# Performance work log

Measured on AMD Instinct MI355X. Metric: run time of the kernel, lower is better.

## Reference

```python
import jax, jax.numpy as jnp
import numpy as np

N, E = 20000, 320000
IN_DIM, CODE_DIM, HIDDEN, HEADS, NREL = 896, 768, 256, 4, 5
CH = HIDDEN // HEADS
CODE_WEIGHT = 3.0
NEG_SLOPE = 0.2


def _gat_layer(h, src, dst, W, att_src, att_dst, bias):
    # h: [N, HIDDEN]; src/dst already include self-loops. Eval mode -> no dropout.
    n = h.shape[0]
    x = (h @ W).reshape(n, HEADS, CH)                      # [N,H,C]
    a_src = (x * att_src).sum(-1)                          # [N,H]
    a_dst = (x * att_dst).sum(-1)                          # [N,H]
    alpha = jax.nn.leaky_relu(a_src[src] + a_dst[dst], NEG_SLOPE)  # [E',H]
    amax = jax.ops.segment_max(alpha, dst, num_segments=n)
    amax = jnp.where(jnp.isfinite(amax), amax, 0.0)
    ex = jnp.exp(alpha - amax[dst])
    denom = jax.ops.segment_sum(ex, dst, num_segments=n)
    coef = ex / denom[dst]                                 # segment softmax over in-neighbors
    msg = x[src] * coef[:, :, None]                        # [E',H,C]
    out = jax.ops.segment_sum(msg, dst, num_segments=n)    # [N,H,C]
    return out.reshape(n, HEADS * CH) + bias


def setup_inputs() -> dict:
    key = jax.random.key(0)
    ks = jax.random.split(key, 20)
    def glorot(k, shape):
        fan_in = shape[0]
        return jax.random.normal(k, shape, jnp.float32) / jnp.sqrt(jnp.asarray(fan_in, jnp.float32))
    inp = {
        "x": jax.random.normal(ks[0], (N, IN_DIM), jnp.float32),
        "edge_index": jax.random.randint(ks[1], (2, E), 0, N, jnp.int32),
        "edge_type": jax.random.randint(ks[2], (E,), 0, NREL, jnp.int32),
        "edge_weight": jax.random.uniform(ks[3], (E,), jnp.float32),
        "rel_emb": jax.random.normal(ks[4], (NREL, HIDDEN), jnp.float32),
        "Wp": glorot(ks[5], (IN_DIM, HIDDEN)),
        "bp": jnp.zeros((HIDDEN,), jnp.float32),
        "W1": glorot(ks[6], (HIDDEN, HIDDEN)),
        "att_src1": glorot(ks[7], (HEADS, CH)) * 0.1,
        "att_dst1": glorot(ks[8], (HEADS, CH)) * 0.1,
        "b1": jnp.zeros((HIDDEN,), jnp.float32),
        "W2": glorot(ks[9], (HIDDEN, HIDDEN)),
        "att_src2": glorot(ks[10], (HEADS, CH)) * 0.1,
        "att_dst2": glorot(ks[11], (HEADS, CH)) * 0.1,
        "b2": jnp.zeros((HIDDEN,), jnp.float32),
        "Wo": glorot(ks[12], (HIDDEN, 1)),
        "bo": jnp.zeros((1,), jnp.float32),
    }
    return inp


def reference(x, edge_index, edge_type, edge_weight, rel_emb, Wp, bp,
              W1, att_src1, att_dst1, b1, W2, att_src2, att_dst2, b2, Wo, bo):
    # feature reorder + code reweighting
    x_code = x[:, :CODE_DIM]
    x_num = x[:, CODE_DIM:]
    xc = jnp.concatenate([x_num, CODE_WEIGHT * x_code], axis=-1)
    h = jax.nn.relu(xc @ Wp + bp)                          # [N,HIDDEN]

    src, dst = edge_index[0], edge_index[1]
    # relational message + index_add scatter
    rel = rel_emb[edge_type] * edge_weight[:, None]        # [E,HIDDEN]
    msg = h[src] + rel
    h = h + jax.ops.segment_sum(msg, dst, num_segments=N)

    # GATConv adds self-loops by default
    loop = jnp.arange(N, dtype=src.dtype)
    src_sl = jnp.concatenate([src, loop])
    dst_sl = jnp.concatenate([dst, loop])

    h = _gat_layer(h, src_sl, dst_sl, W1, att_src1, att_dst1, b1)
    h = _gat_layer(h, src_sl, dst_sl, W2, att_src2, att_dst2, b2)
    score = (h @ Wo + bo)[:, 0]                            # [N]
    return score
```

## Files before the change

### kernel.cpp

```cpp
#include <hip/hip_runtime.h>
#include <hip/hip_bf16.h>

#define N_NODES 20000
#define E_EDGES 320000

typedef __attribute__((ext_vector_type(8))) short s8v;
typedef __attribute__((ext_vector_type(4))) float f4v;

__device__ __forceinline__ float lrelu(float v){ return v > 0.f ? v : 0.2f * v; }

__device__ __forceinline__ float bitf(unsigned short u){
  union { unsigned int i; float f; } v; v.i = ((unsigned int)u) << 16; return v.f;
}
__device__ __forceinline__ float4 bf4(const unsigned short* p){
  ushort4 u = *(const ushort4*)p;
  return make_float4(bitf(u.x), bitf(u.y), bitf(u.z), bitf(u.w));
}
__device__ __forceinline__ unsigned short bfhi(float v){
  union{float f; unsigned u;} a; a.f = v;
  unsigned r = a.u + 0x7FFFu + ((a.u >> 16) & 1u);
  return (unsigned short)(r >> 16);
}
__device__ __forceinline__ float bf2f(unsigned short h){
  union{unsigned u; float f;} a; a.u = ((unsigned)h) << 16; return a.f;
}
__device__ __forceinline__ void split2(float v0, float v1, unsigned& hu, unsigned& lu){
  __hip_bfloat162 h2 = __float22bfloat162_rn(make_float2(v0, v1));
  unsigned h; __builtin_memcpy(&h, &h2, 4);
  union{unsigned u; float f;} c0, c1;
  c0.u = h << 16;
  c1.u = h & 0xFFFF0000u;
  __hip_bfloat162 l2 = __float22bfloat162_rn(make_float2(v0 - c0.f, v1 - c1.f));
  unsigned l; __builtin_memcpy(&l, &l2, 4);
  hu = h; lu = l;
}
__device__ __forceinline__ void gl_lds16(const void* g, void* l){
  __builtin_amdgcn_global_load_lds(
      (const __attribute__((address_space(1))) unsigned int*)g,
      (__attribute__((address_space(3))) unsigned int*)l, 16, 0, 0);
}

__global__ __launch_bounds__(256) void k_count(const int* __restrict__ dst, int* __restrict__ deg, int E){
  int e = blockIdx.x * 256 + threadIdx.x;
  if (e < E) atomicAdd(&deg[dst[e]], 1);
}

__global__ __launch_bounds__(256) void k_scan(const int* __restrict__ deg, int* __restrict__ off,
                                              int* __restrict__ cur, int n){
  __shared__ int part[256];
  __shared__ int base[257];
  int tid = threadIdx.x;
  int chunk = (n + 255) / 256;
  int st = tid * chunk;
  int en = st + chunk; if (en > n) en = n;
  int s = 0;
  for (int i = st; i < en; ++i) s += deg[i];
  part[tid] = s;
  __syncthreads();
  if (tid == 0){
    int a = 0;
    for (int i = 0; i < 256; ++i){ base[i] = a; a += part[i]; }
    base[256] = a;
  }
  __syncthreads();
  int a = base[tid];
  for (int i = st; i < en; ++i){ off[i] = a; cur[i] = 0; a += deg[i]; }
  if (tid == 0) off[n] = base[256];
}

__global__ __launch_bounds__(256) void k_fill(const int* __restrict__ src, const int* __restrict__ dst,
                       const int* __restrict__ ety, const float* __restrict__ ew,
                       const int* __restrict__ off, int* __restrict__ cur,
                       int* __restrict__ csrc, int* __restrict__ cet, float* __restrict__ cw, int E){
  int e = blockIdx.x * 256 + threadIdx.x;
  if (e < E){
    int d = dst[e];
    int p = atomicAdd(&cur[d], 1);
    int i = off[d] + p;
    csrc[i] = src[e];
    cet[i]  = ety[e];
    cw[i]   = ew[e];
  }
}

template<bool SC3>
__global__ __launch_bounds__(64) void k_prep(const float* __restrict__ W, unsigned short* __restrict__ Bp, int K){
  int kt = blockIdx.x;
  int n  = blockIdx.y * 64 + threadIdx.x;
  unsigned short hi[32], lo[32];
#pragma unroll
  for (int kk = 0; kk < 32; ++kk){
    int krow = kt * 32 + kk;
    float v = W[(size_t)krow * 256 + n];
    if constexpr (SC3){ if (krow >= 128) v *= 3.0f; }
    unsigned short h = bfhi(v);
    hi[kk] = h;
    lo[kk] = bfhi(v - bf2f(h));
  }
  size_t plane = (size_t)(K >> 5) * 256 * 32;
  size_t b = ((size_t)kt * 256 + n) * 32;
#pragma unroll
  for (int kk = 0; kk < 32; ++kk){
    Bp[b + kk]         = hi[kk];
    Bp[plane + b + kk] = lo[kk];
  }
}

template<int KT, bool ARAW, bool EPI, bool ATT, bool CBF>
__global__ __launch_bounds__(256, 2) void k_mm(
    const float* __restrict__ Araw,
    const unsigned short* __restrict__ Ahi, const unsigned short* __restrict__ Alo,
    const unsigned short* __restrict__ Bp,
    const float* __restrict__ bias, void* __restrict__ Cout,
    const float* __restrict__ attS, const float* __restrict__ attD,
    float* __restrict__ aS, float* __restrict__ aD)
{
  constexpr int TILE = ARAW ? 8192 : 4096;
  __shared__ alignas(16) unsigned char Abuf[2][TILE];

  const int tid  = threadIdx.x;
  const int lane = tid & 63;
  const int w    = tid >> 6;
  const int l15  = lane & 15;
  const int kg   = lane >> 4;
  const int m0   = blockIdx.x * 32;
  const size_t planeB = (size_t)KT * 256 * 32;

  f4v acc[2][4];
#pragma unroll
  for (int f = 0; f < 2; ++f)
#pragma unroll
    for (int g = 0; g < 4; ++g)
#pragma unroll
      for (int r = 0; r < 4; ++r) acc[f][g][r] = 0.f;

  auto stage = [&](int buf, int kt){
    if constexpr (ARAW){
#pragma unroll
      for (int seg = 0; seg < 2; ++seg){
        int s   = seg * 256 + tid;
        int row = s >> 3;
        int jj  = s & 7;
        int kcp = jj >> 1, h = jj & 1;
        int kc  = kcp ^ (row & 3);
        int c   = kt * 32 + kc * 8 + h * 4;
        int xcol = (c < 128) ? (768 + c) : (c - 128);
        const float* gp = Araw + (size_t)(m0 + row) * 896 + xcol;
        gl_lds16(gp, &Abuf[buf][seg * 4096 + w * 1024]);
      }
    } else {
      int s   = tid;
      int p   = s >> 7;
      int sp  = s & 127;
      int row = sp >> 2;
      int kcp = sp & 3;
      int kc  = kcp ^ (row & 3);
      const unsigned short* basep = p ? Alo : Ahi;
      const unsigned short* gp = basep + (size_t)(m0 + row) * 256 + kt * 32 + kc * 8;
      gl_lds16(gp, &Abuf[buf][w * 1024]);
    }
  };

  auto readFrags = [&](s8v* ah, s8v* al, int buf){
#pragma unroll
    for (int f = 0; f < 2; ++f){
      int row = f * 16 + l15;
      int kc  = kg ^ (row & 3);
      if constexpr (ARAW){
        const unsigned char* p0 = &Abuf[buf][row * 128 + kc * 32];
        float4 x0 = *(const float4*)p0;
        float4 x1 = *(const float4*)(p0 + 16);
        union{unsigned u[4]; s8v s;} H, L;
        split2(x0.x, x0.y, H.u[0], L.u[0]);
        split2(x0.z, x0.w, H.u[1], L.u[1]);
        split2(x1.x, x1.y, H.u[2], L.u[2]);
        split2(x1.z, x1.w, H.u[3], L.u[3]);
        ah[f] = H.s; al[f] = L.s;
      } else {
        ah[f] = *(const s8v*)&Abuf[buf][row * 64 + kc * 16];
        al[f] = *(const s8v*)&Abuf[buf][2048 + row * 64 + kc * 16];
      }
    }
  };

  auto loadB = [&](s8v* bh, s8v* bl, int kt){
#pragma unroll
    for (int g = 0; g < 4; ++g){
      const unsigned short* bp2 = Bp + ((size_t)kt * 256 + w * 64 + g * 16 + l15) * 32 + kg * 8;
      bh[g] = *(const s8v*)bp2;
      bl[g] = *(const s8v*)(bp2 + planeB);
    }
  };

  auto doMFMA = [&](const s8v* ah, const s8v* al, const s8v* bh, const s8v* bl){
#pragma unroll
    for (int f = 0; f < 2; ++f)
#pragma unroll
      for (int g = 0; g < 4; ++g){
        acc[f][g] = __builtin_amdgcn_mfma_f32_16x16x32_bf16(ah[f], bh[g], acc[f][g], 0, 0, 0);
        acc[f][g] = __builtin_amdgcn_mfma_f32_16x16x32_bf16(ah[f], bl[g], acc[f][g], 0, 0, 0);
        acc[f][g] = __builtin_amdgcn_mfma_f32_16x16x32_bf16(al[f], bh[g], acc[f][g], 0, 0, 0);
      }
  };

  s8v bh[4], bl[4];
  stage(0, 0);
  loadB(bh, bl, 0);
  __syncthreads();

  int cur = 0;
#pragma unroll 1
  for (int kt = 0; kt < KT; ++kt){
    if (kt + 1 < KT) stage(cur ^ 1, kt + 1);
    s8v ah[2], al[2];
    readFrags(ah, al, cur);
    s8v nbh[4], nbl[4];
    if (kt + 1 < KT) loadB(nbh, nbl, kt + 1);
    doMFMA(ah, al, bh, bl);
    if (kt + 1 < KT){
#pragma unroll
      for (int g = 0; g < 4; ++g){ bh[g] = nbh[g]; bl[g] = nbl[g]; }
    }
    __syncthreads();
    cur ^= 1;
  }

#pragma unroll
  for (int f = 0; f < 2; ++f){
#pragma unroll
    for (int g = 0; g < 4; ++g){
      int col = w * 64 + g * 16 + l15;
      float bb = EPI ? bias[col] : 0.f;
#pragma unroll
      for (int r = 0; r < 4; ++r){
        int row = m0 + f * 16 + kg * 4 + r;
        float v = acc[f][g][r];
        if constexpr (EPI) v = fmaxf(v + bb, 0.f);
        if constexpr (CBF) ((unsigned short*)Cout)[(size_t)row * 256 + col] = bfhi(v);
        else               ((float*)Cout)[(size_t)row * 256 + col] = v;
      }
    }
  }

  if constexpr (ATT){
    const int head = w;
    float sv[4], dv[4];
#pragma unroll
    for (int g = 0; g < 4; ++g){
      int col = w * 64 + g * 16 + l15;
      sv[g] = attS[col];
      dv[g] = attD[col];
    }
#pragma unroll
    for (int f = 0; f < 2; ++f){
#pragma unroll
      for (int r = 0; r < 4; ++r){
        float ps = acc[f][0][r]*sv[0] + acc[f][1][r]*sv[1] + acc[f][2][r]*sv[2] + acc[f][3][r]*sv[3];
        float pd = acc[f][0][r]*dv[0] + acc[f][1][r]*dv[1] + acc[f][2][r]*dv[2] + acc[f][3][r]*dv[3];
#pragma unroll
        for (int mm = 1; mm < 16; mm <<= 1){
          ps += __shfl_xor(ps, mm, 64);
          pd += __shfl_xor(pd, mm, 64);
        }
        int row = m0 + f * 16 + kg * 4 + r;
        if (l15 == 0){
          aS[(size_t)row * 4 + head] = ps;
          aD[(size_t)row * 4 + head] = pd;
        }
      }
    }
  }
}

__global__ __launch_bounds__(256) void k_agg(
    const unsigned short* __restrict__ h0, const int* __restrict__ off,
    const int* __restrict__ csrc, const int* __restrict__ cet, const float* __restrict__ cw,
    const float* __restrict__ rel,
    unsigned short* __restrict__ h1hi, unsigned short* __restrict__ h1lo, int N)
{
  int n = blockIdx.x * 4 + (threadIdx.x >> 6);
  if (n >= N) return;
  int lane = threadIdx.x & 63;
  int c0 = lane * 4;
  float4 acc = bf4(&h0[(size_t)n * 256 + c0]);
  int s0 = off[n], s1 = off[n + 1];
  int e = s0;
  for (; e + 3 < s1; e += 4){
    int sA = csrc[e], sB = csrc[e+1], sC = csrc[e+2], sD = csrc[e+3];
    int tA = cet[e],  tB = cet[e+1],  tC = cet[e+2],  tD = cet[e+3];
    float wA = cw[e], wB = cw[e+1], wC = cw[e+2], wD = cw[e+3];
    float4 hA = bf4(&h0[(size_t)sA * 256 + c0]);
    float4 hB = bf4(&h0[(size_t)sB * 256 + c0]);
    float4 hC = bf4(&h0[(size_t)sC * 256 + c0]);
    float4 hD = bf4(&h0[(size_t)sD * 256 + c0]);
    float4 rA = *(const float4*)&rel[(size_t)tA * 256 + c0];
    float4 rB = *(const float4*)&rel[(size_t)tB * 256 + c0];
    float4 rC = *(const float4*)&rel[(size_t)tC * 256 + c0];
    float4 rD = *(const float4*)&rel[(size_t)tD * 256 + c0];
    acc.x += hA.x + hB.x + hC.x + hD.x + rA.x*wA + rB.x*wB + rC.x*wC + rD.x*wD;
    acc.y += hA.y + hB.y + hC.y + hD.y + rA.y*wA + rB.y*wB + rC.y*wC + rD.y*wD;
    acc.z += hA.z + hB.z + hC.z + hD.z + rA.z*wA + rB.z*wB + rC.z*wC + rD.z*wD;
    acc.w += hA.w + hB.w + hC.w + hD.w + rA.w*wA + rB.w*wB + rC.w*wC + rD.w*wD;
  }
  for (; e < s1; ++e){
    int s = csrc[e];
    int t = cet[e];
    float wg = cw[e];
    float4 hv = bf4(&h0[(size_t)s * 256 + c0]);
    float4 rv = *(const float4*)&rel[(size_t)t * 256 + c0];
    acc.x += hv.x + rv.x * wg;
    acc.y += hv.y + rv.y * wg;
    acc.z += hv.z + rv.z * wg;
    acc.w += hv.w + rv.w * wg;
  }
  ushort4 hi, lo;
  { unsigned short h;
    h = bfhi(acc.x); hi.x = h; lo.x = bfhi(acc.x - bf2f(h));
    h = bfhi(acc.y); hi.y = h; lo.y = bfhi(acc.y - bf2f(h));
    h = bfhi(acc.z); hi.z = h; lo.z = bfhi(acc.z - bf2f(h));
    h = bfhi(acc.w); hi.w = h; lo.w = bfhi(acc.w - bf2f(h));
  }
  *(ushort4*)&h1hi[(size_t)n * 256 + c0] = hi;
  *(ushort4*)&h1lo[(size_t)n * 256 + c0] = lo;
}

template<bool SCORE>
__global__ __launch_bounds__(256) void k_gat(
    const unsigned short* __restrict__ xh, const float* __restrict__ aS, const float* __restrict__ aD,
    const int* __restrict__ off, const int* __restrict__ csrc,
    const float* __restrict__ bias,
    unsigned short* __restrict__ h1hi, unsigned short* __restrict__ h1lo,
    const float* __restrict__ Wo, const float* __restrict__ bo, float* __restrict__ out, int N)
{
  __shared__ float4 exs[4][128];
  __shared__ int   srcs[4][128];
  const int wv   = threadIdx.x >> 6;
  const int n    = blockIdx.x * 4 + wv;
  if (n >= N) return;
  const int lane = threadIdx.x & 63;
  const int head = lane >> 4;
  const int c0   = lane * 4;
  const int s0 = off[n], s1 = off[n + 1];
  const int deg = s1 - s0;
  const int nc = deg < 128 ? deg : 128;

  float4 ad4 = *(const float4*)&aD[(size_t)n * 4];
  float4 asf = *(const float4*)&aS[(size_t)n * 4];
  float4 aself;
  aself.x = lrelu(asf.x + ad4.x); aself.y = lrelu(asf.y + ad4.y);
  aself.z = lrelu(asf.z + ad4.z); aself.w = lrelu(asf.w + ad4.w);
  float4 q = aself;

  for (int base = 0; base < deg; base += 64){
    int ci = base + lane;
    if (ci < deg){
      int s = csrc[s0 + ci];
      float4 av = *(const float4*)&aS[(size_t)s * 4];
      float4 al4;
      al4.x = lrelu(av.x + ad4.x); al4.y = lrelu(av.y + ad4.y);
      al4.z = lrelu(av.z + ad4.z); al4.w = lrelu(av.w + ad4.w);
      q.x = fmaxf(q.x, al4.x); q.y = fmaxf(q.y, al4.y);
      q.z = fmaxf(q.z, al4.z); q.w = fmaxf(q.w, al4.w);
      if (ci < 128){ srcs[wv][ci] = s; exs[wv][ci] = al4; }
    }
  }
#pragma unroll
  for (int mm = 1; mm < 64; mm <<= 1){
    q.x = fmaxf(q.x, __shfl_xor(q.x, mm, 64));
    q.y = fmaxf(q.y, __shfl_xor(q.y, mm, 64));
    q.z = fmaxf(q.z, __shfl_xor(q.z, mm, 64));
    q.w = fmaxf(q.w, __shfl_xor(q.w, mm, 64));
  }
  asm volatile("s_waitcnt lgkmcnt(0)" ::: "memory");

  float4 den4 = make_float4(0.f, 0.f, 0.f, 0.f);
  for (int ci = lane; ci < nc; ci += 64){
    float4 a = exs[wv][ci];
    float4 e4;
    e4.x = __expf(a.x - q.x); e4.y = __expf(a.y - q.y);
    e4.z = __expf(a.z - q.z); e4.w = __expf(a.w - q.w);
    exs[wv][ci] = e4;
    den4.x += e4.x; den4.y += e4.y; den4.z += e4.z; den4.w += e4.w;
  }
#pragma unroll
  for (int mm = 1; mm < 64; mm <<= 1){
    den4.x += __shfl_xor(den4.x, mm, 64);
    den4.y += __shfl_xor(den4.y, mm, 64);
    den4.z += __shfl_xor(den4.z, mm, 64);
    den4.w += __shfl_xor(den4.w, mm, 64);
  }
  asm volatile("s_waitcnt lgkmcnt(0)" ::: "memory");

  const float mh  = head == 0 ? q.x : (head == 1 ? q.y : (head == 2 ? q.z : q.w));
  const float adh = head == 0 ? ad4.x : (head == 1 ? ad4.y : (head == 2 ? ad4.z : ad4.w));
  const float aselfh = head == 0 ? aself.x : (head == 1 ? aself.y : (head == 2 ? aself.z : aself.w));
  float den = (head == 0 ? den4.x : (head == 1 ? den4.y : (head == 2 ? den4.z : den4.w)));
  float exself = __expf(aselfh - mh);
  den += exself;

  float4 xv = bf4(&xh[(size_t)n * 256 + c0]);
  float4 acc;
  acc.x = exself * xv.x; acc.y = exself * xv.y; acc.z = exself * xv.z; acc.w = exself * xv.w;

  const float* exw = (const float*)&exs[wv][0];
  int e = 0;
  for (; e + 3 < nc; e += 4){
    int sA = srcs[wv][e], sB = srcs[wv][e+1], sC = srcs[wv][e+2], sD = srcs[wv][e+3];
    float eA = exw[(e  ) * 4 + head];
    float eB = exw[(e+1) * 4 + head];
    float eC = exw[(e+2) * 4 + head];
    float eD = exw[(e+3) * 4 + head];
    float4 xA = bf4(&xh[(size_t)sA * 256 + c0]);
    float4 xB = bf4(&xh[(size_t)sB * 256 + c0]);
    float4 xC = bf4(&xh[(size_t)sC * 256 + c0]);
    float4 xD = bf4(&xh[(size_t)sD * 256 + c0]);
    acc.x = fmaf(eA, xA.x, fmaf(eB, xB.x, fmaf(eC, xC.x, fmaf(eD, xD.x, acc.x))));
    acc.y = fmaf(eA, xA.y, fmaf(eB, xB.y, fmaf(eC, xC.y, fmaf(eD, xD.y, acc.y))));
    acc.z = fmaf(eA, xA.z, fmaf(eB, xB.z, fmaf(eC, xC.z, fmaf(eD, xD.z, acc.z))));
    acc.w = fmaf(eA, xA.w, fmaf(eB, xB.w, fmaf(eC, xC.w, fmaf(eD, xD.w, acc.w))));
  }
  for (; e < nc; ++e){
    int s = srcs[wv][e];
    float ef = exw[e * 4 + head];
    float4 x2 = bf4(&xh[(size_t)s * 256 + c0]);
    acc.x = fmaf(ef, x2.x, acc.x);
    acc.y = fmaf(ef, x2.y, acc.y);
    acc.z = fmaf(ef, x2.z, acc.z);
    acc.w = fmaf(ef, x2.w, acc.w);
  }
  for (int ci = 128; ci < deg; ++ci){
    int s = csrc[s0 + ci];
    float a  = aS[(size_t)s * 4 + head];
    float ef = __expf(lrelu(a + adh) - mh);
    den += ef;
    float4 x2 = bf4(&xh[(size_t)s * 256 + c0]);
    acc.x = fmaf(ef, x2.x, acc.x);
    acc.y = fmaf(ef, x2.y, acc.y);
    acc.z = fmaf(ef, x2.z, acc.z);
    acc.w = fmaf(ef, x2.w, acc.w);
  }

  float inv = 1.f / den;
  float4 bb = *(const float4*)&bias[c0];
  float4 o;
  o.x = acc.x * inv + bb.x;
  o.y = acc.y * inv + bb.y;
  o.z = acc.z * inv + bb.z;
  o.w = acc.w * inv + bb.w;
  if constexpr (SCORE){
    float4 wvv = *(const float4*)&Wo[c0];
    float p = o.x * wvv.x + o.y * wvv.y + o.z * wvv.z + o.w * wvv.w;
#pragma unroll
    for (int mm = 1; mm < 64; mm <<= 1) p += __shfl_xor(p, mm, 64);
    if (lane == 0) out[n] = p + bo[0];
  } else {
    ushort4 hi, lo;
    unsigned short h;
    h = bfhi(o.x); hi.x = h; lo.x = bfhi(o.x - bf2f(h));
    h = bfhi(o.y); hi.y = h; lo.y = bfhi(o.y - bf2f(h));
    h = bfhi(o.z); hi.z = h; lo.z = bfhi(o.z - bf2f(h));
    h = bfhi(o.w); hi.w = h; lo.w = bfhi(o.w - bf2f(h));
    *(ushort4*)&h1hi[(size_t)n * 256 + c0] = hi;
    *(ushort4*)&h1lo[(size_t)n * 256 + c0] = lo;
  }
}

extern "C" void kernel_launch(void* const* d_in, const int* in_sizes, int n_in,
                              void* d_out, int out_size, void* d_ws, size_t ws_size,
                              hipStream_t stream)
{
  const float* x   = (const float*)d_in[0];
  const int*   ei  = (const int*)  d_in[1];
  const int*   ety = (const int*)  d_in[2];
  const float* ew  = (const float*)d_in[3];
  const float* rel = (const float*)d_in[4];
  const float* Wp  = (const float*)d_in[5];
  const float* bp  = (const float*)d_in[6];
  const float* W1  = (const float*)d_in[7];
  const float* as1 = (const float*)d_in[8];
  const float* ad1 = (const float*)d_in[9];
  const float* b1  = (const float*)d_in[10];
  const float* W2  = (const float*)d_in[11];
  const float* as2 = (const float*)d_in[12];
  const float* ad2 = (const float*)d_in[13];
  const float* b2  = (const float*)d_in[14];
  const float* Wo  = (const float*)d_in[15];
  const float* bo  = (const float*)d_in[16];
  float* out = (float*)d_out;

  const int N = N_NODES, E = E_EDGES;
  char* w = (char*)d_ws;
  size_t o = 0;
  auto alloc = [&](size_t bytes) -> char* {
    char* p = w + o;
    o = (o + bytes + 255) & ~(size_t)255;
    return p;
  };
  unsigned short* h0b  = (unsigned short*)alloc((size_t)N * 256 * 2);
  unsigned short* xhb  = (unsigned short*)alloc((size_t)N * 256 * 2);
  unsigned short* h1hi = (unsigned short*)alloc((size_t)N * 256 * 2);
  unsigned short* h1lo = (unsigned short*)alloc((size_t)N * 256 * 2);
  float* aS  = (float*)alloc((size_t)N * 4 * 4);
  float* aD  = (float*)alloc((size_t)N * 4 * 4);
  int* deg   = (int*)alloc((size_t)N * 4);
  int* offs  = (int*)alloc((size_t)(N + 1) * 4);
  int* cur   = (int*)alloc((size_t)N * 4);
  int* csrc  = (int*)alloc((size_t)E * 4);
  int* cet   = (int*)alloc((size_t)E * 4);
  float* cw  = (float*)alloc((size_t)E * 4);
  unsigned short* BpP = (unsigned short*)alloc((size_t)2 * 896 * 256 * 2);
  unsigned short* Bp1 = (unsigned short*)alloc((size_t)2 * 256 * 256 * 2);
  unsigned short* Bp2 = (unsigned short*)alloc((size_t)2 * 256 * 256 * 2);

  const int* srcp = ei;
  const int* dstp = ei + E;

  hipMemsetAsync(deg, 0, (size_t)N * 4, stream);
  k_count<<<(E + 255) / 256, 256, 0, stream>>>(dstp, deg, E);
  k_scan<<<1, 256, 0, stream>>>(deg, offs, cur, N);
  k_fill<<<(E + 255) / 256, 256, 0, stream>>>(srcp, dstp, ety, ew, offs, cur, csrc, cet, cw, E);

  k_prep<true ><<<dim3(896 / 32, 4), 64, 0, stream>>>(Wp, BpP, 896);
  k_prep<false><<<dim3(256 / 32, 4), 64, 0, stream>>>(W1, Bp1, 256);
  k_prep<false><<<dim3(256 / 32, 4), 64, 0, stream>>>(W2, Bp2, 256);

  const int gmm = N_NODES / 32;
  int nblk = (N + 3) / 4;

  k_mm<28, true, true, false, true><<<gmm, 256, 0, stream>>>(
      x, nullptr, nullptr, BpP, bp, (void*)h0b, nullptr, nullptr, nullptr, nullptr);
  k_agg<<<nblk, 256, 0, stream>>>(h0b, offs, csrc, cet, cw, rel, h1hi, h1lo, N);
  k_mm<8, false, false, true, true><<<gmm, 256, 0, stream>>>(
      nullptr, h1hi, h1lo, Bp1, nullptr, (void*)xhb, as1, ad1, aS, aD);
  k_gat<false><<<nblk, 256, 0, stream>>>(xhb, aS, aD, offs, csrc, b1, h1hi, h1lo, nullptr, nullptr, nullptr, N);
  k_mm<8, false, false, true, true><<<gmm, 256, 0, stream>>>(
      nullptr, h1hi, h1lo, Bp2, nullptr, (void*)xhb, as2, ad2, aS, aD);
  k_gat<true><<<nblk, 256, 0, stream>>>(xhb, aS, aD, offs, csrc, b2, nullptr, nullptr, Wo, bo, out, N);
}
```

Before: 282.3 us.

## Split projection GEMM by N, reduce relation weights per type, unroll gathers

The input projection gets its own kernel, tiled 32x128 with a 2D grid of 128-thread blocks. It loads fp32 A through registers, applies the code-feature scale there and splits to bf16 hi/lo in LDS, replacing the scale that was folded into the weight prep. The relational aggregation now sums edge weights per relation type with a wave reduction and applies five rel_emb rows once, instead of loading one rel row per edge. It also caches source ids in LDS and unrolls the neighbor gather by 8, and the GAT gather is likewise unrolled by 8 with tree summation. These aim to cut per-edge memory traffic and expose more loads in flight, at the cost of more registers and slightly different rounding.

```diff
diff --git a/kernel.cpp b/kernel.cpp
--- a/kernel.cpp
+++ b/kernel.cpp
@@ -83,16 +83,13 @@
   }
 }
 
-template<bool SC3>
 __global__ __launch_bounds__(64) void k_prep(const float* __restrict__ W, unsigned short* __restrict__ Bp, int K){
   int kt = blockIdx.x;
   int n  = blockIdx.y * 64 + threadIdx.x;
   unsigned short hi[32], lo[32];
 #pragma unroll
   for (int kk = 0; kk < 32; ++kk){
-    int krow = kt * 32 + kk;
-    float v = W[(size_t)krow * 256 + n];
-    if constexpr (SC3){ if (krow >= 128) v *= 3.0f; }
+    float v = W[(size_t)(kt * 32 + kk) * 256 + n];
     unsigned short h = bfhi(v);
     hi[kk] = h;
     lo[kk] = bfhi(v - bf2f(h));
@@ -106,17 +103,114 @@
   }
 }
 
-template<int KT, bool ARAW, bool EPI, bool ATT, bool CBF>
-__global__ __launch_bounds__(256, 2) void k_mm(
-    const float* __restrict__ Araw,
+__global__ __launch_bounds__(128, 4) void k_mmp(
+    const float* __restrict__ A, const unsigned short* __restrict__ Bp,
+    const float* __restrict__ bias, unsigned short* __restrict__ Cout)
+{
+  constexpr int KT = 28;
+  __shared__ unsigned short AhB[2][32 * 40];
+  __shared__ unsigned short AlB[2][32 * 40];
+
+  const int tid  = threadIdx.x;
+  const int lane = tid & 63;
+  const int wn   = tid >> 6;
+  const int l15  = lane & 15;
+  const int kg   = lane >> 4;
+  const int m0   = blockIdx.x * 32;
+  const int n0   = blockIdx.y * 128;
+  const size_t planeB = (size_t)KT * 256 * 32;
+
+  f4v acc[2][4];
+#pragma unroll
+  for (int f = 0; f < 2; ++f)
+#pragma unroll
+    for (int g = 0; g < 4; ++g)
+#pragma unroll
+      for (int r = 0; r < 4; ++r) acc[f][g][r] = 0.f;
+
+  const int arow = tid >> 2;
+  const int aj   = tid & 3;
+  const int gr   = m0 + arow;
+
+  auto loadA = [&](float* v, int kt){
+    int c = kt * 32 + aj * 8;
+    const float* sp; float sc;
+    if (c < 128){ sp = A + (size_t)gr * 896 + (768 + c); sc = 1.f; }
+    else        { sp = A + (size_t)gr * 896 + (c - 128); sc = 3.f; }
+    float4 f0 = *(const float4*)sp;
+    float4 f1 = *(const float4*)(sp + 4);
+    v[0]=f0.x*sc; v[1]=f0.y*sc; v[2]=f0.z*sc; v[3]=f0.w*sc;
+    v[4]=f1.x*sc; v[5]=f1.y*sc; v[6]=f1.z*sc; v[7]=f1.w*sc;
+  };
+  auto writeLDS = [&](const float* v, int buf){
+    union { unsigned u[4]; s8v s; } hv, lv;
+#pragma unroll
+    for (int p = 0; p < 4; ++p)
+      split2(v[2*p], v[2*p+1], hv.u[p], lv.u[p]);
+    *(s8v*)&AhB[buf][arow * 40 + aj * 8] = hv.s;
+    *(s8v*)&AlB[buf][arow * 40 + aj * 8] = lv.s;
+  };
+
+  float av[8];
+  loadA(av, 0);
+  writeLDS(av, 0);
+  loadA(av, 1);
+
+  int cur = 0;
+#pragma unroll 1
+  for (int kt = 0; kt < KT; ++kt){
+    __syncthreads();
+    if (kt + 1 < KT) writeLDS(av, cur ^ 1);
+    if (kt + 2 < KT) loadA(av, kt + 2);
+    s8v bh[4], bl[4];
+#pragma unroll
+    for (int g = 0; g < 4; ++g){
+      const unsigned short* bp2 = Bp + ((size_t)kt * 256 + n0 + wn * 64 + g * 16 + l15) * 32 + kg * 8;
+      bh[g] = *(const s8v*)bp2;
+      bl[g] = *(const s8v*)(bp2 + planeB);
+    }
+    s8v ah[2], al[2];
+#pragma unroll
+    for (int f = 0; f < 2; ++f){
+      int row = f * 16 + l15;
+      ah[f] = *(const s8v*)&AhB[cur][row * 40 + kg * 8];
+      al[f] = *(const s8v*)&AlB[cur][row * 40 + kg * 8];
+    }
+#pragma unroll
+    for (int f = 0; f < 2; ++f)
+#pragma unroll
+      for (int g = 0; g < 4; ++g){
+        acc[f][g] = __builtin_amdgcn_mfma_f32_16x16x32_bf16(ah[f], bh[g], acc[f][g], 0, 0, 0);
+        acc[f][g] = __builtin_amdgcn_mfma_f32_16x16x32_bf16(ah[f], bl[g], acc[f][g], 0, 0, 0);
+        acc[f][g] = __builtin_amdgcn_mfma_f32_16x16x32_bf16(al[f], bh[g], acc[f][g], 0, 0, 0);
+      }
+    cur ^= 1;
+  }
+
+#pragma unroll
+  for (int f = 0; f < 2; ++f){
+#pragma unroll
+    for (int g = 0; g < 4; ++g){
+      int col = n0 + wn * 64 + g * 16 + l15;
+      float bb = bias[col];
+#pragma unroll
+      for (int r = 0; r < 4; ++r){
+        int row = m0 + f * 16 + kg * 4 + r;
+        float v = fmaxf(acc[f][g][r] + bb, 0.f);
+        Cout[(size_t)row * 256 + col] = bfhi(v);
+      }
+    }
+  }
+}
+
+__global__ __launch_bounds__(256, 2) void k_mmh(
     const unsigned short* __restrict__ Ahi, const unsigned short* __restrict__ Alo,
-    const unsigned short* __restrict__ Bp,
-    const float* __restrict__ bias, void* __restrict__ Cout,
+    const unsigned short* __restrict__ Bp, unsigned short* __restrict__ Cout,
     const float* __restrict__ attS, const float* __restrict__ attD,
     float* __restrict__ aS, float* __restrict__ aD)
 {
-  constexpr int TILE = ARAW ? 8192 : 4096;
-  __shared__ alignas(16) unsigned char Abuf[2][TILE];
+  constexpr int KT = 8;
+  __shared__ alignas(16) unsigned char Abuf[2][4096];
 
   const int tid  = threadIdx.x;
   const int lane = tid & 63;
@@ -135,54 +229,25 @@
       for (int r = 0; r < 4; ++r) acc[f][g][r] = 0.f;
 
   auto stage = [&](int buf, int kt){
-    if constexpr (ARAW){
-#pragma unroll
-      for (int seg = 0; seg < 2; ++seg){
-        int s   = seg * 256 + tid;
-        int row = s >> 3;
-        int jj  = s & 7;
-        int kcp = jj >> 1, h = jj & 1;
-        int kc  = kcp ^ (row & 3);
-        int c   = kt * 32 + kc * 8 + h * 4;
-        int xcol = (c < 128) ? (768 + c) : (c - 128);
-        const float* gp = Araw + (size_t)(m0 + row) * 896 + xcol;
-        gl_lds16(gp, &Abuf[buf][seg * 4096 + w * 1024]);
-      }
-    } else {
-      int s   = tid;
-      int p   = s >> 7;
-      int sp  = s & 127;
-      int row = sp >> 2;
-      int kcp = sp & 3;
-      int kc  = kcp ^ (row & 3);
-      const unsigned short* basep = p ? Alo : Ahi;
-      const unsigned short* gp = basep + (size_t)(m0 + row) * 256 + kt * 32 + kc * 8;
-      gl_lds16(gp, &Abuf[buf][w * 1024]);
-    }
+    int s   = tid;
+    int p   = s >> 7;
+    int sp  = s & 127;
+    int row = sp >> 2;
+    int kcp = sp & 3;
+    int kc  = kcp ^ (row & 3);
+    const unsigned short* basep = p ? Alo : Ahi;
+    const unsigned short* gp = basep + (size_t)(m0 + row) * 256 + kt * 32 + kc * 8;
+    gl_lds16(gp, &Abuf[buf][w * 1024]);
   };
-
   auto readFrags = [&](s8v* ah, s8v* al, int buf){
 #pragma unroll
     for (int f = 0; f < 2; ++f){
       int row = f * 16 + l15;
       int kc  = kg ^ (row & 3);
-      if constexpr (ARAW){
-        const unsigned char* p0 = &Abuf[buf][row * 128 + kc * 32];
-        float4 x0 = *(const float4*)p0;
-        float4 x1 = *(const float4*)(p0 + 16);
-        union{unsigned u[4]; s8v s;} H, L;
-        split2(x0.x, x0.y, H.u[0], L.u[0]);
-        split2(x0.z, x0.w, H.u[1], L.u[1]);
-        split2(x1.x, x1.y, H.u[2], L.u[2]);
-        split2(x1.z, x1.w, H.u[3], L.u[3]);
-        ah[f] = H.s; al[f] = L.s;
-      } else {
-        ah[f] = *(const s8v*)&Abuf[buf][row * 64 + kc * 16];
-        al[f] = *(const s8v*)&Abuf[buf][2048 + row * 64 + kc * 16];
-      }
+      ah[f] = *(const s8v*)&Abuf[buf][row * 64 + kc * 16];
+      al[f] = *(const s8v*)&Abuf[buf][2048 + row * 64 + kc * 16];
     }
   };
-
   auto loadB = [&](s8v* bh, s8v* bl, int kt){
 #pragma unroll
     for (int g = 0; g < 4; ++g){
@@ -191,7 +256,6 @@
       bl[g] = *(const s8v*)(bp2 + planeB);
     }
   };
-
   auto doMFMA = [&](const s8v* ah, const s8v* al, const s8v* bh, const s8v* bl){
 #pragma unroll
     for (int f = 0; f < 2; ++f)
@@ -230,19 +294,15 @@
 #pragma unroll
     for (int g = 0; g < 4; ++g){
       int col = w * 64 + g * 16 + l15;
-      float bb = EPI ? bias[col] : 0.f;
 #pragma unroll
       for (int r = 0; r < 4; ++r){
         int row = m0 + f * 16 + kg * 4 + r;
-        float v = acc[f][g][r];
-        if constexpr (EPI) v = fmaxf(v + bb, 0.f);
-        if constexpr (CBF) ((unsigned short*)Cout)[(size_t)row * 256 + col] = bfhi(v);
-        else               ((float*)Cout)[(size_t)row * 256 + col] = v;
+        Cout[(size_t)row * 256 + col] = bfhi(acc[f][g][r]);
       }
     }
   }
 
-  if constexpr (ATT){
+  {
     const int head = w;
     float sv[4], dv[4];
 #pragma unroll
@@ -278,41 +338,87 @@
     const float* __restrict__ rel,
     unsigned short* __restrict__ h1hi, unsigned short* __restrict__ h1lo, int N)
 {
-  int n = blockIdx.x * 4 + (threadIdx.x >> 6);
+  __shared__ int srcs[4][128];
+  const int wv = threadIdx.x >> 6;
+  const int n  = blockIdx.x * 4 + wv;
   if (n >= N) return;
-  int lane = threadIdx.x & 63;
-  int c0 = lane * 4;
+  const int lane = threadIdx.x & 63;
+  const int c0 = lane * 4;
+  const int s0 = off[n], s1 = off[n + 1];
+  const int deg = s1 - s0;
+  const int nc = deg < 128 ? deg : 128;
+
+  float w0=0.f, w1=0.f, w2=0.f, w3=0.f, w4=0.f;
+  for (int base = 0; base < deg; base += 64){
+    int ci = base + lane;
+    if (ci < deg){
+      int e = s0 + ci;
+      int s = csrc[e];
+      int t = cet[e];
+      float wg = cw[e];
+      if (ci < 128) srcs[wv][ci] = s;
+      w0 += (t == 0) ? wg : 0.f;
+      w1 += (t == 1) ? wg : 0.f;
+      w2 += (t == 2) ? wg : 0.f;
+      w3 += (t == 3) ? wg : 0.f;
+      w4 += (t == 4) ? wg : 0.f;
+    }
+  }
+#pragma unroll
+  for (int mm = 1; mm < 64; mm <<= 1){
+    w0 += __shfl_xor(w0, mm, 64);
+    w1 += __shfl_xor(w1, mm, 64);
+    w2 += __shfl_xor(w2, mm, 64);
+    w3 += __shfl_xor(w3, mm, 64);
+    w4 += __shfl_xor(w4, mm, 64);
+  }
+  asm volatile("s_waitcnt lgkmcnt(0)" ::: "memory");
+
   float4 acc = bf4(&h0[(size_t)n * 256 + c0]);
-  int s0 = off[n], s1 = off[n + 1];
-  int e = s0;
-  for (; e + 3 < s1; e += 4){
-    int sA = csrc[e], sB = csrc[e+1], sC = csrc[e+2], sD = csrc[e+3];
-    int tA = cet[e],  tB = cet[e+1],  tC = cet[e+2],  tD = cet[e+3];
-    float wA = cw[e], wB = cw[e+1], wC = cw[e+2], wD = cw[e+3];
-    float4 hA = bf4(&h0[(size_t)sA * 256 + c0]);
-    float4 hB = bf4(&h0[(size_t)sB * 256 + c0]);
-    float4 hC = bf4(&h0[(size_t)sC * 256 + c0]);
-    float4 hD = bf4(&h0[(size_t)sD * 256 + c0]);
-    float4 rA = *(const float4*)&rel[(size_t)tA * 256 + c0];
-    float4 rB = *(const float4*)&rel[(size_t)tB * 256 + c0];
-    float4 rC = *(const float4*)&rel[(size_t)tC * 256 + c0];
-    float4 rD = *(const float4*)&rel[(size_t)tD * 256 + c0];
-    acc.x += hA.x + hB.x + hC.x + hD.x + rA.x*wA + rB.x*wB + rC.x*wC + rD.x*wD;
-    acc.y += hA.y + hB.y + hC.y + hD.y + rA.y*wA + rB.y*wB + rC.y*wC + rD.y*wD;
-    acc.z += hA.z + hB.z + hC.z + hD.z + rA.z*wA + rB.z*wB + rC.z*wC + rD.z*wD;
-    acc.w += hA.w + hB.w + hC.w + hD.w + rA.w*wA + rB.w*wB + rC.w*wC + rD.w*wD;
-  }
-  for (; e < s1; ++e){
-    int s = csrc[e];
-    int t = cet[e];
-    float wg = cw[e];
-    float4 hv = bf4(&h0[(size_t)s * 256 + c0]);
-    float4 rv = *(const float4*)&rel[(size_t)t * 256 + c0];
-    acc.x += hv.x + rv.x * wg;
-    acc.y += hv.y + rv.y * wg;
-    acc.z += hv.z + rv.z * wg;
-    acc.w += hv.w + rv.w * wg;
-  }
+  { float4 R = *(const float4*)&rel[0 * 256 + c0];
+    acc.x = fmaf(w0, R.x, acc.x); acc.y = fmaf(w0, R.y, acc.y);
+    acc.z = fmaf(w0, R.z, acc.z); acc.w = fmaf(w0, R.w, acc.w); }
+  { float4 R = *(const float4*)&rel[1 * 256 + c0];
+    acc.x = fmaf(w1, R.x, acc.x); acc.y = fmaf(w1, R.y, acc.y);
+    acc.z = fmaf(w1, R.z, acc.z); acc.w = fmaf(w1, R.w, acc.w); }
+  { float4 R = *(const float4*)&rel[2 * 256 + c0];
+    acc.x = fmaf(w2, R.x, acc.x); acc.y = fmaf(w2, R.y, acc.y);
+    acc.z = fmaf(w2, R.z, acc.z); acc.w = fmaf(w2, R.w, acc.w); }
+  { float4 R = *(const float4*)&rel[3 * 256 + c0];
+    acc.x = fmaf(w3, R.x, acc.x); acc.y = fmaf(w3, R.y, acc.y);
+    acc.z = fmaf(w3, R.z, acc.z); acc.w = fmaf(w3, R.w, acc.w); }
+  { float4 R = *(const float4*)&rel[4 * 256 + c0];
+    acc.x = fmaf(w4, R.x, acc.x); acc.y = fmaf(w4, R.y, acc.y);
+    acc.z = fmaf(w4, R.z, acc.z); acc.w = fmaf(w4, R.w, acc.w); }
+
+  int e = 0;
+  for (; e + 7 < nc; e += 8){
+    int sA = srcs[wv][e  ], sB = srcs[wv][e+1], sC = srcs[wv][e+2], sD = srcs[wv][e+3];
+    int sE = srcs[wv][e+4], sF = srcs[wv][e+5], sG = srcs[wv][e+6], sH = srcs[wv][e+7];
+    float4 xA = bf4(&h0[(size_t)sA * 256 + c0]);
+    float4 xB = bf4(&h0[(size_t)sB * 256 + c0]);
+    float4 xC = bf4(&h0[(size_t)sC * 256 + c0]);
+    float4 xD = bf4(&h0[(size_t)sD * 256 + c0]);
+    float4 xE = bf4(&h0[(size_t)sE * 256 + c0]);
+    float4 xF = bf4(&h0[(size_t)sF * 256 + c0]);
+    float4 xG = bf4(&h0[(size_t)sG * 256 + c0]);
+    float4 xH = bf4(&h0[(size_t)sH * 256 + c0]);
+    acc.x += ((xA.x + xB.x) + (xC.x + xD.x)) + ((xE.x + xF.x) + (xG.x + xH.x));
+    acc.y += ((xA.y + xB.y) + (xC.y + xD.y)) + ((xE.y + xF.y) + (xG.y + xH.y));
+    acc.z += ((xA.z + xB.z) + (xC.z + xD.z)) + ((xE.z + xF.z) + (xG.z + xH.z));
+    acc.w += ((xA.w + xB.w) + (xC.w + xD.w)) + ((xE.w + xF.w) + (xG.w + xH.w));
+  }
+  for (; e < nc; ++e){
+    int s = srcs[wv][e];
+    float4 xv = bf4(&h0[(size_t)s * 256 + c0]);
+    acc.x += xv.x; acc.y += xv.y; acc.z += xv.z; acc.w += xv.w;
+  }
+  for (int ci = 128; ci < deg; ++ci){
+    int s = csrc[s0 + ci];
+    float4 xv = bf4(&h0[(size_t)s * 256 + c0]);
+    acc.x += xv.x; acc.y += xv.y; acc.z += xv.z; acc.w += xv.w;
+  }
+
   ushort4 hi, lo;
   { unsigned short h;
     h = bfhi(acc.x); hi.x = h; lo.x = bfhi(acc.x - bf2f(h));
@@ -404,20 +510,30 @@
 
   const float* exw = (const float*)&exs[wv][0];
   int e = 0;
-  for (; e + 3 < nc; e += 4){
-    int sA = srcs[wv][e], sB = srcs[wv][e+1], sC = srcs[wv][e+2], sD = srcs[wv][e+3];
-    float eA = exw[(e  ) * 4 + head];
-    float eB = exw[(e+1) * 4 + head];
-    float eC = exw[(e+2) * 4 + head];
-    float eD = exw[(e+3) * 4 + head];
+  for (; e + 7 < nc; e += 8){
+    int sA = srcs[wv][e  ], sB = srcs[wv][e+1], sC = srcs[wv][e+2], sD = srcs[wv][e+3];
+    int sE = srcs[wv][e+4], sF = srcs[wv][e+5], sG = srcs[wv][e+6], sH = srcs[wv][e+7];
+    float eA = exw[(e  ) * 4 + head], eB = exw[(e+1) * 4 + head];
+    float eC = exw[(e+2) * 4 + head], eD = exw[(e+3) * 4 + head];
+    float eE = exw[(e+4) * 4 + head], eF = exw[(e+5) * 4 + head];
+    float eG = exw[(e+6) * 4 + head], eH = exw[(e+7) * 4 + head];
     float4 xA = bf4(&xh[(size_t)sA * 256 + c0]);
     float4 xB = bf4(&xh[(size_t)sB * 256 + c0]);
     float4 xC = bf4(&xh[(size_t)sC * 256 + c0]);
     float4 xD = bf4(&xh[(size_t)sD * 256 + c0]);
-    acc.x = fmaf(eA, xA.x, fmaf(eB, xB.x, fmaf(eC, xC.x, fmaf(eD, xD.x, acc.x))));
-    acc.y = fmaf(eA, xA.y, fmaf(eB, xB.y, fmaf(eC, xC.y, fmaf(eD, xD.y, acc.y))));
-    acc.z = fmaf(eA, xA.z, fmaf(eB, xB.z, fmaf(eC, xC.z, fmaf(eD, xD.z, acc.z))));
-    acc.w = fmaf(eA, xA.w, fmaf(eB, xB.w, fmaf(eC, xC.w, fmaf(eD, xD.w, acc.w))));
+    float4 xE = bf4(&xh[(size_t)sE * 256 + c0]);
+    float4 xF = bf4(&xh[(size_t)sF * 256 + c0]);
+    float4 xG = bf4(&xh[(size_t)sG * 256 + c0]);
+    float4 xH = bf4(&xh[(size_t)sH * 256 + c0]);
+    float t0, t1, t2, t3;
+    t0 = eA*xA.x + eB*xB.x; t1 = eC*xC.x + eD*xD.x; t2 = eE*xE.x + eF*xF.x; t3 = eG*xG.x + eH*xH.x;
+    acc.x += (t0 + t1) + (t2 + t3);
+    t0 = eA*xA.y + eB*xB.y; t1 = eC*xC.y + eD*xD.y; t2 = eE*xE.y + eF*xF.y; t3 = eG*xG.y + eH*xH.y;
+    acc.y += (t0 + t1) + (t2 + t3);
+    t0 = eA*xA.z + eB*xB.z; t1 = eC*xC.z + eD*xD.z; t2 = eE*xE.z + eF*xF.z; t3 = eG*xG.z + eH*xH.z;
+    acc.z += (t0 + t1) + (t2 + t3);
+    t0 = eA*xA.w + eB*xB.w; t1 = eC*xC.w + eD*xD.w; t2 = eE*xE.w + eF*xF.w; t3 = eG*xG.w + eH*xH.w;
+    acc.w += (t0 + t1) + (t2 + t3);
   }
   for (; e < nc; ++e){
     int s = srcs[wv][e];
@@ -520,20 +636,17 @@
   k_scan<<<1, 256, 0, stream>>>(deg, offs, cur, N);
   k_fill<<<(E + 255) / 256, 256, 0, stream>>>(srcp, dstp, ety, ew, offs, cur, csrc, cet, cw, E);
 
-  k_prep<true ><<<dim3(896 / 32, 4), 64, 0, stream>>>(Wp, BpP, 896);
-  k_prep<false><<<dim3(256 / 32, 4), 64, 0, stream>>>(W1, Bp1, 256);
-  k_prep<false><<<dim3(256 / 32, 4), 64, 0, stream>>>(W2, Bp2, 256);
+  k_prep<<<dim3(896 / 32, 4), 64, 0, stream>>>(Wp, BpP, 896);
+  k_prep<<<dim3(256 / 32, 4), 64, 0, stream>>>(W1, Bp1, 256);
+  k_prep<<<dim3(256 / 32, 4), 64, 0, stream>>>(W2, Bp2, 256);
 
   const int gmm = N_NODES / 32;
   int nblk = (N + 3) / 4;
 
-  k_mm<28, true, true, false, true><<<gmm, 256, 0, stream>>>(
-      x, nullptr, nullptr, BpP, bp, (void*)h0b, nullptr, nullptr, nullptr, nullptr);
+  k_mmp<<<dim3(gmm, 2), 128, 0, stream>>>(x, BpP, bp, h0b);
   k_agg<<<nblk, 256, 0, stream>>>(h0b, offs, csrc, cet, cw, rel, h1hi, h1lo, N);
-  k_mm<8, false, false, true, true><<<gmm, 256, 0, stream>>>(
-      nullptr, h1hi, h1lo, Bp1, nullptr, (void*)xhb, as1, ad1, aS, aD);
+  k_mmh<<<gmm, 256, 0, stream>>>(h1hi, h1lo, Bp1, xhb, as1, ad1, aS, aD);
   k_gat<false><<<nblk, 256, 0, stream>>>(xhb, aS, aD, offs, csrc, b1, h1hi, h1lo, nullptr, nullptr, nullptr, N);
-  k_mm<8, false, false, true, true><<<gmm, 256, 0, stream>>>(
-      nullptr, h1hi, h1lo, Bp2, nullptr, (void*)xhb, as2, ad2, aS, aD);
+  k_mmh<<<gmm, 256, 0, stream>>>(h1hi, h1lo, Bp2, xhb, as2, ad2, aS, aD);
   k_gat<true><<<nblk, 256, 0, stream>>>(xhb, aS, aD, offs, csrc, b2, nullptr, nullptr, Wo, bo, out, N);
 }
```

Result: faster. 276.6 us (-2.0%).
